# Performance work log

Hardware: AMD Instinct MI355X
Metric: run time of the kernel (lower is better)

## Reference

```python
import jax, jax.numpy as jnp
import numpy as np

B, S, D, H = 8, 1024, 768, 12
DH = D // H  # per-head dim = 64


def setup_inputs() -> dict:
    key = jax.random.key(0)
    ks = jax.random.split(key, 9)
    scale = 1.0 / np.sqrt(D)
    x = jax.random.normal(ks[0], (B, S, D), dtype=jnp.float32)
    # Per-head projection weights stacked over the head axis [H, D, DH]
    Wq = jax.random.normal(ks[1], (H, D, DH), dtype=jnp.float32) * scale
    bq = jax.random.normal(ks[2], (H, DH), dtype=jnp.float32) * 0.02
    Wk = jax.random.normal(ks[3], (H, D, DH), dtype=jnp.float32) * scale
    bk = jax.random.normal(ks[4], (H, DH), dtype=jnp.float32) * 0.02
    Wv = jax.random.normal(ks[5], (H, D, DH), dtype=jnp.float32) * scale
    bv = jax.random.normal(ks[6], (H, DH), dtype=jnp.float32) * 0.02
    Wo = jax.random.normal(ks[7], (D, D), dtype=jnp.float32) * scale
    bo = jax.random.normal(ks[8], (D,), dtype=jnp.float32) * 0.02
    return {"x": x, "Wq": Wq, "bq": bq, "Wk": Wk, "bk": bk,
            "Wv": Wv, "bv": bv, "Wo": Wo, "bo": bo}


def reference(x, Wq, bq, Wk, bk, Wv, bv, Wo, bo):
    # Batched equivalent of the per-head Python loop: each head has its own
    # Q/K/V linear projections (weights stacked on the head axis).
    q = jnp.einsum('bsd,hde->bhse', x, Wq) + bq[None, :, None, :]
    k = jnp.einsum('bsd,hde->bhse', x, Wk) + bk[None, :, None, :]
    v = jnp.einsum('bsd,hde->bhse', x, Wv) + bv[None, :, None, :]
    scores = jnp.einsum('bhse,bhte->bhst', q, k) / jnp.sqrt(jnp.float32(DH))
    attn = jax.nn.softmax(scores, axis=-1)
    out = jnp.einsum('bhst,bhte->bhse', attn, v)  # [B,H,S,DH]
    # concat heads on last dim -> [B,S,H*DH] = [B,S,D]
    out = out.transpose(0, 2, 1, 3).reshape(B, S, D)
    return out @ Wo.T + bo
```

## Files before the change

### kernel.cpp

```cpp
#include <hip/hip_runtime.h>
#include <hip/hip_bf16.h>


typedef unsigned short u16;
typedef unsigned int u32;
typedef __attribute__((ext_vector_type(8))) short bf16x8;
typedef __attribute__((ext_vector_type(8))) unsigned short u16x8;
typedef __attribute__((ext_vector_type(4))) float f32x4;
typedef __attribute__((ext_vector_type(4))) u32 u32x4;

typedef __attribute__((address_space(1))) const u32* gas_u32;
typedef __attribute__((address_space(3))) u32* las_u32;

#define DEVI __device__ __forceinline__

DEVI u16 f2bf(float f) {
  union { float f; u32 u; } v; v.f = f;
  u32 r = v.u + 0x7fffu + ((v.u >> 16) & 1u);
  return (u16)(r >> 16);
}

DEVI void gll16(const void* g, void* l) {
  __builtin_amdgcn_global_load_lds((gas_u32)g, (las_u32)l, 16, 0, 0);
}

DEVI f32x4 mfma16(bf16x8 a, bf16x8 b, f32x4 c) {
  return __builtin_amdgcn_mfma_f32_16x16x32_bf16(a, b, c, 0, 0, 0);
}

DEVI u32 cvtpk(float lo, float hi) {
  u32 r;
  asm("v_cvt_pk_bf16_f32 %0, %1, %2" : "=v"(r) : "v"(lo), "v"(hi));
  return r;
}

__global__ __launch_bounds__(256) void k_conv(const float* __restrict__ in,
                                              u16* __restrict__ out, int n4) {
  int i = blockIdx.x * 256 + threadIdx.x;
  if (i >= n4) return;
  float4 v = ((const float4*)in)[i];
  ushort4 o;
  o.x = f2bf(v.x); o.y = f2bf(v.y); o.z = f2bf(v.z); o.w = f2bf(v.w);
  ((ushort4*)out)[i] = o;
}

__global__ __launch_bounds__(256) void k_transW(const float* __restrict__ Wq,
                                                const float* __restrict__ Wk,
                                                const float* __restrict__ Wv,
                                                u16* __restrict__ Wtb) {
  __shared__ u16 T[64][65];
  const int th = blockIdx.y;
  const float* W = (th < 12) ? Wq : (th < 24) ? Wk : Wv;
  const int h = th % 12;
  W += (size_t)h * 768 * 64;
  const int k0 = blockIdx.x * 64;
  const int tid = threadIdx.x;
  const int row = tid >> 2, c = tid & 3;
  const float* src = W + (size_t)(k0 + row) * 64 + c * 16;
#pragma unroll
  for (int j = 0; j < 4; ++j) {
    float4 v = ((const float4*)src)[j];
    T[row][c * 16 + j * 4 + 0] = f2bf(v.x);
    T[row][c * 16 + j * 4 + 1] = f2bf(v.y);
    T[row][c * 16 + j * 4 + 2] = f2bf(v.z);
    T[row][c * 16 + j * 4 + 3] = f2bf(v.w);
  }
  __syncthreads();
  const int e = tid >> 2;
  u16* dst = Wtb + ((size_t)th * 64 + e) * 768 + k0 + c * 16;
  alignas(16) u16 tmp[16];
#pragma unroll
  for (int j = 0; j < 16; ++j) tmp[j] = T[c * 16 + j][e];
  *(u16x8*)(dst)     = *(const u16x8*)(tmp);
  *(u16x8*)(dst + 8) = *(const u16x8*)(tmp + 8);
}

template <int MODE>
__global__ __launch_bounds__(256) void k_gemm(const u16* __restrict__ Ab,
                                              const u16* __restrict__ Bb,
                                              const float* __restrict__ bias,
                                              void* __restrict__ outp) {
  __shared__ u16 smem[12288];
  u16* As = smem;
  u16* Bs = smem + 128 * 64;
  const int tid = threadIdx.x;
  const int w = tid >> 6, lane = tid & 63, lq = lane & 15, g = lane >> 4;
  const int wm = w >> 1, wn = w & 1;
  const int m0 = blockIdx.x * 128;
  const int pn = blockIdx.y;
  const u16* Brows = Bb + (size_t)pn * 64 * 768;

  f32x4 acc[4][2];
#pragma unroll
  for (int mf = 0; mf < 4; ++mf)
#pragma unroll
    for (int nf = 0; nf < 2; ++nf) acc[mf][nf] = (f32x4){0.f, 0.f, 0.f, 0.f};

  for (int kt = 0; kt < 12; ++kt) {
    const int kb = kt * 64;
#pragma unroll
    for (int i = 0; i < 4; ++i) {
      int c = w * 4 + i;
      int id = c * 64 + lane;
      int row = id >> 3, cb = id & 7;
      gll16(Ab + (size_t)(m0 + row) * 768 + kb + ((cb ^ (row & 7)) << 3), As + c * 512);
    }
#pragma unroll
    for (int i = 0; i < 2; ++i) {
      int c = w * 2 + i;
      int id = c * 64 + lane;
      int row = id >> 3, cb = id & 7;
      gll16(Brows + (size_t)row * 768 + kb + ((cb ^ (row & 7)) << 3), Bs + c * 512);
    }
    __syncthreads();
#pragma unroll
    for (int kk = 0; kk < 2; ++kk) {
      bf16x8 a[4], b[2];
#pragma unroll
      for (int mf = 0; mf < 4; ++mf) {
        int row = wm * 64 + mf * 16 + lq;
        a[mf] = *(const bf16x8*)(As + row * 64 + (((kk * 64 + g * 16) ^ ((row & 7) << 4)) >> 1));
      }
#pragma unroll
      for (int nf = 0; nf < 2; ++nf) {
        int row = wn * 32 + nf * 16 + lq;
        b[nf] = *(const bf16x8*)(Bs + row * 64 + (((kk * 64 + g * 16) ^ ((row & 7) << 4)) >> 1));
      }
#pragma unroll
      for (int mf = 0; mf < 4; ++mf)
#pragma unroll
        for (int nf = 0; nf < 2; ++nf)
          acc[mf][nf] = mfma16(a[mf], b[nf], acc[mf][nf]);
    }
    __syncthreads();
  }

  if (MODE == 2) {
    u16* Ct = smem;
#pragma unroll
    for (int nf = 0; nf < 2; ++nf) {
      const int e = wn * 32 + nf * 16 + lq;
      const float bi = bias[pn * 64 + e];
#pragma unroll
      for (int mf = 0; mf < 4; ++mf)
#pragma unroll
        for (int r = 0; r < 4; ++r) {
          int sl = wm * 64 + mf * 16 + 4 * g + r;
          Ct[e * 136 + sl] = f2bf(acc[mf][nf][r] + bi);
        }
    }
    __syncthreads();
    const int b = m0 >> 10;
    const int er = tid >> 2, cc = tid & 3;
    u16* dst = (u16*)outp + ((size_t)(b * 12 + pn) * 64 + er) * 1024 + (m0 & 1023) + cc * 32;
#pragma unroll
    for (int i = 0; i < 4; ++i)
      *(u16x8*)(dst + i * 8) = *(const u16x8*)(Ct + er * 136 + cc * 32 + i * 8);
  } else {
    float* out = (float*)outp;
#pragma unroll
    for (int nf = 0; nf < 2; ++nf) {
      const int n = pn * 64 + wn * 32 + nf * 16 + lq;
      const float bi = bias[n];
#pragma unroll
      for (int mf = 0; mf < 4; ++mf)
#pragma unroll
        for (int r = 0; r < 4; ++r) {
          int m = m0 + wm * 64 + mf * 16 + 4 * g + r;
          out[(size_t)m * 768 + n] = acc[mf][nf][r] + bi;
        }
    }
  }
}

__global__ __launch_bounds__(256) void k_gemmQK(const u16* __restrict__ Ab,
                                                const u16* __restrict__ Bb,
                                                const float* __restrict__ b0,
                                                const float* __restrict__ b1,
                                                u16* __restrict__ outp) {
  __shared__ u16 smem[16384];
  u16* As = smem;
  u16* Bs = smem + 8192;
  const int tid = threadIdx.x;
  const int w = tid >> 6, lane = tid & 63, lq = lane & 15, g = lane >> 4;
  const int wm = w >> 1, wn = w & 1;
  const int pm = blockIdx.x, pn = blockIdx.y;
  const int m0 = pm * 128;
  const u16* Arows = Ab + (size_t)m0 * 768;
  const u16* Brows = Bb + (size_t)pn * 128 * 768;

  f32x4 acc[4][4];
#pragma unroll
  for (int mf = 0; mf < 4; ++mf)
#pragma unroll
    for (int nf = 0; nf < 4; ++nf) acc[mf][nf] = (f32x4){0.f, 0.f, 0.f, 0.f};

  for (int kt = 0; kt < 12; ++kt) {
    const int kb = kt * 64;
#pragma unroll
    for (int i = 0; i < 4; ++i) {
      int c = w * 4 + i;
      int id = c * 64 + lane;
      int row = id >> 3, cb = id & 7;
      int sw = (cb ^ (row & 7)) << 3;
      gll16(Arows + (size_t)row * 768 + kb + sw, As + c * 512);
      gll16(Brows + (size_t)row * 768 + kb + sw, Bs + c * 512);
    }
    __syncthreads();
#pragma unroll
    for (int kk = 0; kk < 2; ++kk) {
      bf16x8 a[4], b[4];
#pragma unroll
      for (int mf = 0; mf < 4; ++mf) {
        int row = wm * 64 + mf * 16 + lq;
        a[mf] = *(const bf16x8*)(As + row * 64 + (((kk * 64 + g * 16) ^ ((row & 7) << 4)) >> 1));
      }
#pragma unroll
      for (int nf = 0; nf < 4; ++nf) {
        int row = wn * 64 + nf * 16 + lq;
        b[nf] = *(const bf16x8*)(Bs + row * 64 + (((kk * 64 + g * 16) ^ ((row & 7) << 4)) >> 1));
      }
#pragma unroll
      for (int mf = 0; mf < 4; ++mf)
#pragma unroll
        for (int nf = 0; nf < 4; ++nf)
          acc[mf][nf] = mfma16(a[mf], b[nf], acc[mf][nf]);
    }
    __syncthreads();
  }

  const int t = (pn >= 6) ? 1 : 0;
  const float qs = t ? 1.0f : 0.18033688f;
  const float* bp = t ? b1 : b0;
  const int pn6 = pn - t * 6;
  u16* out = outp + (size_t)t * 6291456;
  const int b = m0 >> 10;
#pragma unroll
  for (int nf = 0; nf < 4; ++nf) {
    const int n = pn6 * 128 + wn * 64 + nf * 16 + lq;
    const int h = n >> 6, e = n & 63;
    const float bi = bp[n];
#pragma unroll
    for (int mf = 0; mf < 4; ++mf)
#pragma unroll
      for (int r = 0; r < 4; ++r) {
        int s = (m0 & 1023) + wm * 64 + mf * 16 + 4 * g + r;
        out[((size_t)(b * 12 + h) << 16) + s * 64 + e] = f2bf((acc[mf][nf][r] + bi) * qs);
      }
  }
}

__global__ __launch_bounds__(512) void k_attn(const u16* __restrict__ Qb,
                                              const u16* __restrict__ Kb,
                                              const u16* __restrict__ VTb,
                                              u16* __restrict__ AO) {
  __shared__ u16 Ksm[2][4096];
  __shared__ u16 Vsm[2][4096];
  const int tid = threadIdx.x;
  const int w = tid >> 6, lane = tid & 63, lq = lane & 15, g = lane >> 4;
  const int bh = blockIdx.y, b = bh / 12, h = bh % 12;
  const int q0 = blockIdx.x * 128 + w * 16;
  const u16* Qw = Qb + ((size_t)bh * 1024 + q0) * 64;
  const u16* Kp = Kb + (size_t)bh * 65536;
  const u16* Vp = VTb + (size_t)bh * 65536;
  const bool gsel = (g & 1);

  bf16x8 qf[2];
#pragma unroll
  for (int kk = 0; kk < 2; ++kk)
    qf[kk] = *(const bf16x8*)(Qw + lq * 64 + kk * 32 + g * 8);

  f32x4 o[4];
#pragma unroll
  for (int ef = 0; ef < 4; ++ef) o[ef] = (f32x4){0.f, 0.f, 0.f, 0.f};
  float l_ = 0.f;

#define STAGE(buf, kt_)                                                          \
  {                                                                              \
    const int kb_ = (kt_) * 64;                                                  \
    const int id = w * 64 + lane;                                                \
    const int row = id >> 3, cb = id & 7;                                        \
    const int sb = cb ^ (row & 7);                                               \
    const int tb = (sb & 4) | ((sb & 1) << 1) | ((sb >> 1) & 1);                 \
    gll16(Kp + (size_t)(kb_ + row) * 64 + (sb << 3), &Ksm[buf][w * 512]);        \
    gll16(Vp + (size_t)row * 1024 + kb_ + (tb << 3), &Vsm[buf][w * 512]);        \
  }

#define TILE(buf)                                                                \
  {                                                                              \
    f32x4 s[4];                                                                  \
    _Pragma("unroll")                                                            \
    for (int kf = 0; kf < 4; ++kf) s[kf] = (f32x4){0.f, 0.f, 0.f, 0.f};          \
    __builtin_amdgcn_s_setprio(1);                                               \
    _Pragma("unroll")                                                            \
    for (int kf = 0; kf < 4; ++kf) {                                             \
      const int row = kf * 16 + lq;                                              \
      _Pragma("unroll")                                                          \
      for (int kk = 0; kk < 2; ++kk) {                                           \
        bf16x8 kfr = *(const bf16x8*)(&Ksm[buf][0] + row * 64 +                  \
                                      (((kk * 64 + g * 16) ^ ((row & 7) << 4)) >> 1)); \
        s[kf] = mfma16(kfr, qf[kk], s[kf]);                                      \
      }                                                                          \
    }                                                                            \
    __builtin_amdgcn_s_setprio(0);                                               \
    float sm = 0.f;                                                              \
    _Pragma("unroll")                                                            \
    for (int kf = 0; kf < 4; ++kf)                                               \
      _Pragma("unroll")                                                          \
      for (int r = 0; r < 4; ++r) {                                              \
        float p = __builtin_amdgcn_exp2f(s[kf][r]);                              \
        s[kf][r] = p;                                                            \
        sm += p;                                                                 \
      }                                                                          \
    l_ += sm;                                                                    \
    u32 D[4][2];                                                                 \
    _Pragma("unroll")                                                            \
    for (int kf = 0; kf < 4; ++kf) {                                             \
      D[kf][0] = cvtpk(s[kf][0], s[kf][1]);                                      \
      D[kf][1] = cvtpk(s[kf][2], s[kf][3]);                                      \
    }                                                                            \
    _Pragma("unroll")                                                            \
    for (int kk = 0; kk < 2; ++kk) {                                             \
      const int kk2 = kk * 2;                                                    \
      u32 sa0 = gsel ? D[kk2][0] : D[kk2 + 1][0];                                \
      u32 sa1 = gsel ? D[kk2][1] : D[kk2 + 1][1];                                \
      u32 xa0 = __shfl_xor(sa0, 16), xa1 = __shfl_xor(sa1, 16);                  \
      u32x4 t = { gsel ? xa0 : D[kk2][0],                                        \
                  gsel ? xa1 : D[kk2][1],                                        \
                  gsel ? D[kk2 + 1][0] : xa0,                                    \
                  gsel ? D[kk2 + 1][1] : xa1 };                                  \
      bf16x8 pb = __builtin_bit_cast(bf16x8, t);                                 \
      __builtin_amdgcn_s_setprio(1);                                             \
      _Pragma("unroll")                                                          \
      for (int ef = 0; ef < 4; ++ef) {                                           \
        const int row = ef * 16 + lq;                                            \
        bf16x8 vf = *(const bf16x8*)(&Vsm[buf][0] + row * 64 +                   \
                                     (((kk * 64 + g * 16) ^ ((row & 7) << 4)) >> 1)); \
        o[ef] = mfma16(vf, pb, o[ef]);                                           \
      }                                                                          \
      __builtin_amdgcn_s_setprio(0);                                             \
    }                                                                            \
  }

  STAGE(0, 0)
  asm volatile("s_waitcnt vmcnt(0)" ::: "memory");
  __syncthreads();

  for (int it = 0; it < 8; ++it) {
    const int kt = it * 2;
    STAGE(1, kt + 1)
    TILE(0)
    asm volatile("s_waitcnt vmcnt(0)" ::: "memory");
    __syncthreads();
    if (it < 7) STAGE(0, kt + 2)
    TILE(1)
    asm volatile("s_waitcnt vmcnt(0)" ::: "memory");
    __syncthreads();
  }

  l_ += __shfl_xor(l_, 16);
  l_ += __shfl_xor(l_, 32);

  const float inv = 1.0f / l_;
  u16* dst = AO + ((size_t)(b * 1024 + q0 + lq)) * 768 + h * 64 + g * 4;
#pragma unroll
  for (int ef = 0; ef < 4; ++ef) {
    ushort4 t;
    t.x = f2bf(o[ef][0] * inv);
    t.y = f2bf(o[ef][1] * inv);
    t.z = f2bf(o[ef][2] * inv);
    t.w = f2bf(o[ef][3] * inv);
    *(ushort4*)(dst + ef * 16) = t;
  }
#undef STAGE
#undef TILE
}

extern "C" void kernel_launch(void* const* d_in, const int* in_sizes, int n_in,
                              void* d_out, int out_size, void* d_ws, size_t ws_size,
                              hipStream_t stream) {
  (void)in_sizes; (void)n_in; (void)out_size; (void)ws_size;
  const float* x  = (const float*)d_in[0];
  const float* Wq = (const float*)d_in[1];
  const float* bq = (const float*)d_in[2];
  const float* Wk = (const float*)d_in[3];
  const float* bk = (const float*)d_in[4];
  const float* Wv = (const float*)d_in[5];
  const float* bv = (const float*)d_in[6];
  const float* Wo = (const float*)d_in[7];
  const float* bo = (const float*)d_in[8];

  char* ws = (char*)d_ws;
  u16* xb  = (u16*)(ws);
  u16* Wtb = (u16*)(ws + 12582912);
  u16* Wob = (u16*)(ws + 12582912 + 3538944);
  u16* Qb  = (u16*)(ws + 12582912 + 3538944 + 1179648);
  u16* Kb  = Qb + (size_t)96 * 1024 * 64;
  u16* VTb = Kb + (size_t)96 * 1024 * 64;
  u16* AO  = xb;

  k_conv<<<6291456 / 1024, 256, 0, stream>>>(x, xb, 6291456 / 4);
  k_conv<<<589824 / 1024, 256, 0, stream>>>(Wo, Wob, 589824 / 4);
  k_transW<<<dim3(12, 36), 256, 0, stream>>>(Wq, Wk, Wv, Wtb);

  k_gemmQK<<<dim3(64, 12), 256, 0, stream>>>(xb, Wtb, bq, bk, Qb);
  k_gemm<2><<<dim3(64, 12), 256, 0, stream>>>(xb, Wtb + (size_t)2 * 589824, bv, (void*)VTb);

  k_attn<<<dim3(8, 96), 512, 0, stream>>>(Qb, Kb, VTb, AO);

  k_gemm<3><<<dim3(64, 12), 256, 0, stream>>>(AO, Wob, bo, d_out);
}
```

Before: 123.1 us.

## Process two query tiles per wave in attention to reuse K/V fragments

Halves the attention block to 256 threads (4 waves) and has each wave handle 32 query rows as two 16-row tiles. Each K and V fragment read from LDS now feeds two MFMAs, which halves LDS read traffic per unit of compute. Each wave issues two global-to-LDS loads per stage instead of one. The cost is higher register pressure from doubled accumulators and fewer waves per block, which may reduce latency hiding.

```diff
diff --git a/kernel.cpp b/kernel.cpp
--- a/kernel.cpp
+++ b/kernel.cpp
@@ -250,7 +250,7 @@
   }
 }
 
-__global__ __launch_bounds__(512) void k_attn(const u16* __restrict__ Qb,
+__global__ __launch_bounds__(256) void k_attn(const u16* __restrict__ Qb,
                                               const u16* __restrict__ Kb,
                                               const u16* __restrict__ VTb,
                                               u16* __restrict__ AO) {
@@ -259,38 +259,48 @@
   const int tid = threadIdx.x;
   const int w = tid >> 6, lane = tid & 63, lq = lane & 15, g = lane >> 4;
   const int bh = blockIdx.y, b = bh / 12, h = bh % 12;
-  const int q0 = blockIdx.x * 128 + w * 16;
+  const int q0 = blockIdx.x * 128 + w * 32;
   const u16* Qw = Qb + ((size_t)bh * 1024 + q0) * 64;
   const u16* Kp = Kb + (size_t)bh * 65536;
   const u16* Vp = VTb + (size_t)bh * 65536;
   const bool gsel = (g & 1);
 
-  bf16x8 qf[2];
-#pragma unroll
-  for (int kk = 0; kk < 2; ++kk)
-    qf[kk] = *(const bf16x8*)(Qw + lq * 64 + kk * 32 + g * 8);
-
-  f32x4 o[4];
-#pragma unroll
-  for (int ef = 0; ef < 4; ++ef) o[ef] = (f32x4){0.f, 0.f, 0.f, 0.f};
-  float l_ = 0.f;
+  bf16x8 qf[2][2];
+#pragma unroll
+  for (int nq = 0; nq < 2; ++nq)
+#pragma unroll
+    for (int kk = 0; kk < 2; ++kk)
+      qf[nq][kk] = *(const bf16x8*)(Qw + (nq * 16 + lq) * 64 + kk * 32 + g * 8);
+
+  f32x4 o[2][4];
+#pragma unroll
+  for (int nq = 0; nq < 2; ++nq)
+#pragma unroll
+    for (int ef = 0; ef < 4; ++ef) o[nq][ef] = (f32x4){0.f, 0.f, 0.f, 0.f};
+  float l0 = 0.f, l1 = 0.f;
 
 #define STAGE(buf, kt_)                                                          \
   {                                                                              \
     const int kb_ = (kt_) * 64;                                                  \
-    const int id = w * 64 + lane;                                                \
-    const int row = id >> 3, cb = id & 7;                                        \
-    const int sb = cb ^ (row & 7);                                               \
-    const int tb = (sb & 4) | ((sb & 1) << 1) | ((sb >> 1) & 1);                 \
-    gll16(Kp + (size_t)(kb_ + row) * 64 + (sb << 3), &Ksm[buf][w * 512]);        \
-    gll16(Vp + (size_t)row * 1024 + kb_ + (tb << 3), &Vsm[buf][w * 512]);        \
+    _Pragma("unroll")                                                            \
+    for (int i = 0; i < 2; ++i) {                                                \
+      int c = w * 2 + i;                                                         \
+      int id = c * 64 + lane;                                                    \
+      int row = id >> 3, cb = id & 7;                                            \
+      int sb = cb ^ (row & 7);                                                   \
+      int tb = (sb & 4) | ((sb & 1) << 1) | ((sb >> 1) & 1);                     \
+      gll16(Kp + (size_t)(kb_ + row) * 64 + (sb << 3), &Ksm[buf][c * 512]);      \
+      gll16(Vp + (size_t)row * 1024 + kb_ + (tb << 3), &Vsm[buf][c * 512]);      \
+    }                                                                            \
   }
 
 #define TILE(buf)                                                                \
   {                                                                              \
-    f32x4 s[4];                                                                  \
-    _Pragma("unroll")                                                            \
-    for (int kf = 0; kf < 4; ++kf) s[kf] = (f32x4){0.f, 0.f, 0.f, 0.f};          \
+    f32x4 s[2][4];                                                               \
+    _Pragma("unroll")                                                            \
+    for (int nq = 0; nq < 2; ++nq)                                               \
+      _Pragma("unroll")                                                          \
+      for (int kf = 0; kf < 4; ++kf) s[nq][kf] = (f32x4){0.f, 0.f, 0.f, 0.f};    \
     __builtin_amdgcn_s_setprio(1);                                               \
     _Pragma("unroll")                                                            \
     for (int kf = 0; kf < 4; ++kf) {                                             \
@@ -299,44 +309,57 @@
       for (int kk = 0; kk < 2; ++kk) {                                           \
         bf16x8 kfr = *(const bf16x8*)(&Ksm[buf][0] + row * 64 +                  \
                                       (((kk * 64 + g * 16) ^ ((row & 7) << 4)) >> 1)); \
-        s[kf] = mfma16(kfr, qf[kk], s[kf]);                                      \
+        s[0][kf] = mfma16(kfr, qf[0][kk], s[0][kf]);                             \
+        s[1][kf] = mfma16(kfr, qf[1][kk], s[1][kf]);                             \
       }                                                                          \
     }                                                                            \
     __builtin_amdgcn_s_setprio(0);                                               \
-    float sm = 0.f;                                                              \
+    float sm0 = 0.f, sm1 = 0.f;                                                  \
     _Pragma("unroll")                                                            \
     for (int kf = 0; kf < 4; ++kf)                                               \
       _Pragma("unroll")                                                          \
       for (int r = 0; r < 4; ++r) {                                              \
-        float p = __builtin_amdgcn_exp2f(s[kf][r]);                              \
-        s[kf][r] = p;                                                            \
-        sm += p;                                                                 \
+        float p0 = __builtin_amdgcn_exp2f(s[0][kf][r]);                          \
+        float p1 = __builtin_amdgcn_exp2f(s[1][kf][r]);                          \
+        s[0][kf][r] = p0; s[1][kf][r] = p1;                                      \
+        sm0 += p0; sm1 += p1;                                                    \
       }                                                                          \
-    l_ += sm;                                                                    \
-    u32 D[4][2];                                                                 \
+    l0 += sm0; l1 += sm1;                                                        \
+    u32 D0[4][2], D1[4][2];                                                      \
     _Pragma("unroll")                                                            \
     for (int kf = 0; kf < 4; ++kf) {                                             \
-      D[kf][0] = cvtpk(s[kf][0], s[kf][1]);                                      \
-      D[kf][1] = cvtpk(s[kf][2], s[kf][3]);                                      \
+      D0[kf][0] = cvtpk(s[0][kf][0], s[0][kf][1]);                               \
+      D0[kf][1] = cvtpk(s[0][kf][2], s[0][kf][3]);                               \
+      D1[kf][0] = cvtpk(s[1][kf][0], s[1][kf][1]);                               \
+      D1[kf][1] = cvtpk(s[1][kf][2], s[1][kf][3]);                               \
     }                                                                            \
     _Pragma("unroll")                                                            \
     for (int kk = 0; kk < 2; ++kk) {                                             \
       const int kk2 = kk * 2;                                                    \
-      u32 sa0 = gsel ? D[kk2][0] : D[kk2 + 1][0];                                \
-      u32 sa1 = gsel ? D[kk2][1] : D[kk2 + 1][1];                                \
+      u32 sa0 = gsel ? D0[kk2][0] : D0[kk2 + 1][0];                              \
+      u32 sa1 = gsel ? D0[kk2][1] : D0[kk2 + 1][1];                              \
+      u32 sb0 = gsel ? D1[kk2][0] : D1[kk2 + 1][0];                              \
+      u32 sb1 = gsel ? D1[kk2][1] : D1[kk2 + 1][1];                              \
       u32 xa0 = __shfl_xor(sa0, 16), xa1 = __shfl_xor(sa1, 16);                  \
-      u32x4 t = { gsel ? xa0 : D[kk2][0],                                        \
-                  gsel ? xa1 : D[kk2][1],                                        \
-                  gsel ? D[kk2 + 1][0] : xa0,                                    \
-                  gsel ? D[kk2 + 1][1] : xa1 };                                  \
-      bf16x8 pb = __builtin_bit_cast(bf16x8, t);                                 \
+      u32 xb0 = __shfl_xor(sb0, 16), xb1 = __shfl_xor(sb1, 16);                  \
+      u32x4 t0 = { gsel ? xa0 : D0[kk2][0],                                      \
+                   gsel ? xa1 : D0[kk2][1],                                      \
+                   gsel ? D0[kk2 + 1][0] : xa0,                                  \
+                   gsel ? D0[kk2 + 1][1] : xa1 };                                \
+      u32x4 t1 = { gsel ? xb0 : D1[kk2][0],                                      \
+                   gsel ? xb1 : D1[kk2][1],                                      \
+                   gsel ? D1[kk2 + 1][0] : xb0,                                  \
+                   gsel ? D1[kk2 + 1][1] : xb1 };                                \
+      bf16x8 pb0 = __builtin_bit_cast(bf16x8, t0);                               \
+      bf16x8 pb1 = __builtin_bit_cast(bf16x8, t1);                               \
       __builtin_amdgcn_s_setprio(1);                                             \
       _Pragma("unroll")                                                          \
       for (int ef = 0; ef < 4; ++ef) {                                           \
         const int row = ef * 16 + lq;                                            \
         bf16x8 vf = *(const bf16x8*)(&Vsm[buf][0] + row * 64 +                   \
                                      (((kk * 64 + g * 16) ^ ((row & 7) << 4)) >> 1)); \
-        o[ef] = mfma16(vf, pb, o[ef]);                                           \
+        o[0][ef] = mfma16(vf, pb0, o[0][ef]);                                    \
+        o[1][ef] = mfma16(vf, pb1, o[1][ef]);                                    \
       }                                                                          \
       __builtin_amdgcn_s_setprio(0);                                             \
     }                                                                            \
@@ -358,19 +381,22 @@
     __syncthreads();
   }
 
-  l_ += __shfl_xor(l_, 16);
-  l_ += __shfl_xor(l_, 32);
-
-  const float inv = 1.0f / l_;
-  u16* dst = AO + ((size_t)(b * 1024 + q0 + lq)) * 768 + h * 64 + g * 4;
-#pragma unroll
-  for (int ef = 0; ef < 4; ++ef) {
-    ushort4 t;
-    t.x = f2bf(o[ef][0] * inv);
-    t.y = f2bf(o[ef][1] * inv);
-    t.z = f2bf(o[ef][2] * inv);
-    t.w = f2bf(o[ef][3] * inv);
-    *(ushort4*)(dst + ef * 16) = t;
+  l0 += __shfl_xor(l0, 16); l0 += __shfl_xor(l0, 32);
+  l1 += __shfl_xor(l1, 16); l1 += __shfl_xor(l1, 32);
+
+#pragma unroll
+  for (int nq = 0; nq < 2; ++nq) {
+    const float inv = 1.0f / (nq ? l1 : l0);
+    u16* dst = AO + ((size_t)(b * 1024 + q0 + nq * 16 + lq)) * 768 + h * 64 + g * 4;
+#pragma unroll
+    for (int ef = 0; ef < 4; ++ef) {
+      ushort4 t;
+      t.x = f2bf(o[nq][ef][0] * inv);
+      t.y = f2bf(o[nq][ef][1] * inv);
+      t.z = f2bf(o[nq][ef][2] * inv);
+      t.w = f2bf(o[nq][ef][3] * inv);
+      *(ushort4*)(dst + ef * 16) = t;
+    }
   }
 #undef STAGE
 #undef TILE
@@ -406,7 +432,7 @@
   k_gemmQK<<<dim3(64, 12), 256, 0, stream>>>(xb, Wtb, bq, bk, Qb);
   k_gemm<2><<<dim3(64, 12), 256, 0, stream>>>(xb, Wtb + (size_t)2 * 589824, bv, (void*)VTb);
 
-  k_attn<<<dim3(8, 96), 512, 0, stream>>>(Qb, Kb, VTb, AO);
+  k_attn<<<dim3(8, 96), 256, 0, stream>>>(Qb, Kb, VTb, AO);
 
   k_gemm<3><<<dim3(64, 12), 256, 0, stream>>>(AO, Wob, bo, d_out);
 }
```

Result: slower. 127.4 us (+3.5%).
